# Optimization experiments

Measured on AMD Instinct MI355X. Metric: run time of the kernel, lower is better.

The kernel has to match this reference:

```python
import jax, jax.numpy as jnp
import numpy as np

V, E, H, D = 10000, 256, 512, 768  # vocab, embed, hidden(=attn), encoder dims
B, T, N = 32, 128, 196


def setup_inputs() -> dict:
    key = jax.random.key(0)
    ks = jax.random.split(key, 16)
    s = 0.02
    inp = {
        "x": jax.random.randint(ks[0], (B, T), 0, V),
        "enc_mem": jax.random.normal(ks[1], (B, N, D), dtype=jnp.float32),
        "enc_mask": jnp.ones((B, N), dtype=jnp.int32),
        # parameters, stored (in, out) so y = x @ W
        "emb_table": jax.random.normal(ks[2], (V, E), dtype=jnp.float32) * s,
        "We": jax.random.normal(ks[3], (D, H), dtype=jnp.float32) * s,   # attn.W_e
        "Wh": jax.random.normal(ks[4], (H, H), dtype=jnp.float32) * s,   # attn.W_h
        "v": jax.random.normal(ks[5], (H,), dtype=jnp.float32) * s,      # attn.v
        "Wih": jax.random.normal(ks[6], (E + D, 4 * H), dtype=jnp.float32) * s,
        "Whh": jax.random.normal(ks[7], (H, 4 * H), dtype=jnp.float32) * s,
        "bih": jnp.zeros((4 * H,), dtype=jnp.float32),
        "bhh": jnp.zeros((4 * H,), dtype=jnp.float32),
        "fcW": jax.random.normal(ks[8], (H, V), dtype=jnp.float32) * s,
        "fcb": jnp.zeros((V,), dtype=jnp.float32),
        "W2h": jax.random.normal(ks[9], (D, H), dtype=jnp.float32) * s,  # enc_to_h
        "b2h": jnp.zeros((H,), dtype=jnp.float32),
        "W2c": jax.random.normal(ks[10], (D, H), dtype=jnp.float32) * s,  # enc_to_c
        "b2c": jnp.zeros((H,), dtype=jnp.float32),
    }
    return inp


def _decode(x, enc_mem, enc_mask, emb_table, We, Wh, v, Wih, Whh, bih, bhh,
            fcW, fcb, W2h, b2h, W2c, b2c):
    emb = emb_table[x]                       # (B,T,E); dropout=0 (eval)
    pooled = enc_mem.mean(axis=1)            # (B,D)
    h = jnp.tanh(pooled @ W2h + b2h)         # init_hidden
    c = jnp.tanh(pooled @ W2c + b2c)
    Ke = jnp.einsum('bnd,dh->bnh', enc_mem, We)  # precompute W_e(enc_mem)
    neg = jnp.float32(-1e9)
    mask0 = (enc_mask == 0)

    def step(carry, e_t):
        h, c = carry
        energy = jnp.tanh((h @ Wh)[:, None, :] + Ke)        # (B,N,H)
        scores = jnp.einsum('bnh,h->bn', energy, v)         # (B,N)
        scores = jnp.where(mask0, neg, scores)
        alpha = jax.nn.softmax(scores, axis=-1)
        context = jnp.einsum('bn,bnd->bd', alpha, enc_mem)  # (B,D)
        lstm_in = jnp.concatenate([e_t, context], axis=-1)  # (B,E+D)
        gates = lstm_in @ Wih + bih + h @ Whh + bhh         # (B,4H)
        i_g, f_g, g_g, o_g = jnp.split(gates, 4, axis=-1)   # torch order i,f,g,o
        c_new = jax.nn.sigmoid(f_g) * c + jax.nn.sigmoid(i_g) * jnp.tanh(g_g)
        h_new = jax.nn.sigmoid(o_g) * jnp.tanh(c_new)
        logit = h_new @ fcW + fcb                           # (B,V)
        return (h_new, c_new), logit

    (h, c), logits_t = jax.lax.scan(step, (h, c), jnp.swapaxes(emb, 0, 1))
    logits = jnp.swapaxes(logits_t, 0, 1)                   # (B,T,V)
    return logits, h, c


def reference(x, enc_mem, enc_mask, emb_table, We, Wh, v, Wih, Whh, bih, bhh,
              fcW, fcb, W2h, b2h, W2c, b2c):
    return _decode(x, enc_mem, enc_mask, emb_table, We, Wh, v, Wih, Whh,
                   bih, bhh, fcW, fcb, W2h, b2h, W2c, b2c)
```

## Files before the change

### kernel.cpp

```cpp
#include <hip/hip_runtime.h>

typedef unsigned short u16;
typedef __attribute__((ext_vector_type(8))) short short8;
typedef __attribute__((ext_vector_type(4))) float f32x4;
typedef __attribute__((ext_vector_type(4))) unsigned int u32x4;

#define B_  32
#define T_  128
#define N_  196
#define D_  768
#define E_  256
#define H_  512
#define V_  10000
#define G4H 2048
#define NBLK 256
#define BH  (B_ * H_)
#define BD  (B_ * D_)

#define O_ENCBF 0UL
#define O_WHT   9633792UL
#define O_WHHT  10158080UL
#define O_WIHDT 12255232UL
#define O_KE    15400960UL
#define O_GEMB  21823488UL
#define O_BSUM  38600704UL
#define O_CT    38608896UL
#define O_HIST  38674432UL
#define O_HX2   42868736UL
#define O_HWX   42934272UL
#define O_CTXA  42999808UL
#define O_DEN   43196416UL
#define O_BARS  43196672UL
#define O_REL   43198720UL

__device__ __forceinline__ float b2f(u16 u) {
  union { unsigned i; float f; } c; c.i = ((unsigned)u) << 16; return c.f;
}
__device__ __forceinline__ u16 f2b(float f) {
  unsigned u = __float_as_uint(f);
  unsigned r = (u + 0x7fffu + ((u >> 16) & 1u)) >> 16;
  return (u16)r;
}
__device__ __forceinline__ float fast_tanh(float x) {
  float e = __expf(2.f * x);
  return 1.f - 2.f * __builtin_amdgcn_rcpf(e + 1.f);
}
__device__ __forceinline__ float sigm(float x) {
  return __builtin_amdgcn_rcpf(1.f + __expf(-x));
}
__device__ __forceinline__ float wred_sum(float x) {
  #pragma unroll
  for (int o = 32; o; o >>= 1) x += __shfl_xor(x, o, 64);
  return x;
}

__device__ __forceinline__ float ld_bypass_f32(const float* p) {
  float v;
  asm volatile("global_load_dword %0, %1, off sc0 sc1\n\ts_waitcnt vmcnt(0)"
               : "=v"(v) : "v"(p) : "memory");
  return v;
}
__device__ __forceinline__ unsigned ld_bypass_u32(const unsigned* p) {
  unsigned v;
  asm volatile("global_load_dword %0, %1, off sc0 sc1\n\ts_waitcnt vmcnt(0)"
               : "=v"(v) : "v"(p) : "memory");
  return v;
}
__device__ __forceinline__ void ld2_bypass(const void* p0, const void* p1,
                                           u32x4& a, u32x4& b) {
  asm volatile(
    "global_load_dwordx4 %0, %2, off sc0 sc1\n\t"
    "global_load_dwordx4 %1, %3, off sc0 sc1\n\t"
    "s_waitcnt vmcnt(0)"
    : "=&v"(a), "=&v"(b) : "v"(p0), "v"(p1) : "memory");
}
__device__ __forceinline__ void ld6_1_bypass(
    const void* p0, const void* p1, const void* p2, const void* p3,
    const void* p4, const void* p5, const void* pd,
    u32x4& a, u32x4& b, u32x4& c, u32x4& d, u32x4& e, u32x4& f, float& dv) {
  asm volatile(
    "global_load_dwordx4 %0, %7, off sc0 sc1\n\t"
    "global_load_dwordx4 %1, %8, off sc0 sc1\n\t"
    "global_load_dwordx4 %2, %9, off sc0 sc1\n\t"
    "global_load_dwordx4 %3, %10, off sc0 sc1\n\t"
    "global_load_dwordx4 %4, %11, off sc0 sc1\n\t"
    "global_load_dwordx4 %5, %12, off sc0 sc1\n\t"
    "global_load_dword %6, %13, off sc0 sc1\n\t"
    "s_waitcnt vmcnt(0)"
    : "=&v"(a), "=&v"(b), "=&v"(c), "=&v"(d), "=&v"(e), "=&v"(f), "=&v"(dv)
    : "v"(p0), "v"(p1), "v"(p2), "v"(p3), "v"(p4), "v"(p5), "v"(pd)
    : "memory");
}
__device__ __forceinline__ void st_bypass_f32(float* p, float v) {
  asm volatile("global_store_dword %0, %1, off sc0 sc1" :: "v"(p), "v"(v) : "memory");
}
__device__ __forceinline__ void st_bypass_u32(unsigned* p, unsigned v) {
  asm volatile("global_store_dword %0, %1, off sc0 sc1" :: "v"(p), "v"(v) : "memory");
}
__device__ __forceinline__ void st_bypass_u16(u16* p, u16 v) {
  unsigned vv = v;
  asm volatile("global_store_short %0, %1, off sc0 sc1" :: "v"(p), "v"(vv) : "memory");
}

__device__ __forceinline__ unsigned bar_sum16(const unsigned* p) {
  unsigned a0,a1,a2,a3,a4,a5,a6,a7,a8,a9,a10,a11,a12,a13,a14,a15;
  asm volatile(
    "global_load_dword %0, %16, off sc0 sc1\n\t"
    "global_load_dword %1, %16, off offset:128 sc0 sc1\n\t"
    "global_load_dword %2, %16, off offset:256 sc0 sc1\n\t"
    "global_load_dword %3, %16, off offset:384 sc0 sc1\n\t"
    "global_load_dword %4, %16, off offset:512 sc0 sc1\n\t"
    "global_load_dword %5, %16, off offset:640 sc0 sc1\n\t"
    "global_load_dword %6, %16, off offset:768 sc0 sc1\n\t"
    "global_load_dword %7, %16, off offset:896 sc0 sc1\n\t"
    "global_load_dword %8, %16, off offset:1024 sc0 sc1\n\t"
    "global_load_dword %9, %16, off offset:1152 sc0 sc1\n\t"
    "global_load_dword %10, %16, off offset:1280 sc0 sc1\n\t"
    "global_load_dword %11, %16, off offset:1408 sc0 sc1\n\t"
    "global_load_dword %12, %16, off offset:1536 sc0 sc1\n\t"
    "global_load_dword %13, %16, off offset:1664 sc0 sc1\n\t"
    "global_load_dword %14, %16, off offset:1792 sc0 sc1\n\t"
    "global_load_dword %15, %16, off offset:1920 sc0 sc1\n\t"
    "s_waitcnt vmcnt(0)"
    : "=&v"(a0), "=&v"(a1), "=&v"(a2), "=&v"(a3), "=&v"(a4), "=&v"(a5),
      "=&v"(a6), "=&v"(a7), "=&v"(a8), "=&v"(a9), "=&v"(a10), "=&v"(a11),
      "=&v"(a12), "=&v"(a13), "=&v"(a14), "=&v"(a15)
    : "v"(p) : "memory");
  return ((a0+a1)+(a2+a3)) + ((a4+a5)+(a6+a7)) +
         ((a8+a9)+(a10+a11)) + ((a12+a13)+(a14+a15));
}

__device__ __forceinline__ void gridbar(unsigned* bars, unsigned* rel,
                                        int bid, unsigned target) {
  __syncthreads();
  if (bid == 0) {
    if (threadIdx.x == 0) {
      asm volatile("s_waitcnt vmcnt(0) lgkmcnt(0)" ::: "memory");
      __hip_atomic_fetch_add(bars, 1u, __ATOMIC_RELAXED, __HIP_MEMORY_SCOPE_AGENT);
      while (bar_sum16(bars) < target) __builtin_amdgcn_s_sleep(1);
    }
    __syncthreads();
    if (threadIdx.x < NBLK) st_bypass_u32(rel + (size_t)threadIdx.x * 32, target);
  } else {
    if (threadIdx.x == 0) {
      asm volatile("s_waitcnt vmcnt(0) lgkmcnt(0)" ::: "memory");
      __hip_atomic_fetch_add(bars + (size_t)(bid & 15) * 32, 1u,
                             __ATOMIC_RELAXED, __HIP_MEMORY_SCOPE_AGENT);
      while (ld_bypass_u32(rel + (size_t)bid * 32) < target)
        __builtin_amdgcn_s_sleep(2);
    }
    __syncthreads();
  }
}


__global__ void conv_bf(const float* __restrict__ in, u16* __restrict__ out, int n) {
  int i = blockIdx.x * blockDim.x + threadIdx.x;
  int st = gridDim.x * blockDim.x;
  for (; i < n; i += st) out[i] = f2b(in[i]);
}

__global__ void bsum_k(const float* __restrict__ a, const float* __restrict__ b,
                       float* __restrict__ o, int n) {
  int i = blockIdx.x * blockDim.x + threadIdx.x;
  if (i < n) o[i] = a[i] + b[i];
}

__global__ void transpose_bf(const float* __restrict__ in, u16* __restrict__ out, int R, int C) {
  __shared__ float tl[64][65];
  int tid = threadIdx.x;
  int tc0 = blockIdx.x * 64, tr0 = blockIdx.y * 64;
  int cc = tid & 63;
  for (int rr = tid >> 6; rr < 64; rr += 4) {
    int rg = tr0 + rr, cg = tc0 + cc;
    tl[rr][cc] = (rg < R && cg < C) ? in[(size_t)rg * C + cg] : 0.f;
  }
  __syncthreads();
  int rr = tid & 63;
  for (int c2 = tid >> 6; c2 < 64; c2 += 4) {
    int cg = tc0 + c2, rg = tr0 + rr;
    if (cg < C && rg < R) out[(size_t)cg * R + rg] = f2b(tl[rr][c2]);
  }
}

__global__ __launch_bounds__(512) void init_hc(
    const float* __restrict__ enc, const float* __restrict__ W2h,
    const float* __restrict__ b2h, const float* __restrict__ W2c,
    const float* __restrict__ b2c, u16* __restrict__ hx2, float* __restrict__ cT)
{
  __shared__ float pool[D_];
  int b = blockIdx.x, tid = threadIdx.x;
  for (int d = tid; d < D_; d += 512) {
    float s = 0.f;
    const float* ep = enc + (size_t)b * N_ * D_ + d;
    for (int n = 0; n < N_; ++n) s += ep[(size_t)n * D_];
    pool[d] = s * (1.f / 196.f);
  }
  __syncthreads();
  float a = b2h[tid], a2 = b2c[tid];
  #pragma unroll 4
  for (int d = 0; d < D_; ++d) {
    float pv = pool[d];
    a  += pv * W2h[d * H_ + tid];
    a2 += pv * W2c[d * H_ + tid];
  }
  hx2[b * H_ + tid] = f2b(fast_tanh(a));
  cT[b * H_ + tid] = fast_tanh(a2);
}

template<int AMODE, int OUTMODE, int BIAS>
__global__ __launch_bounds__(256) void gemm2(
    const void* __restrict__ Av, const float* __restrict__ Bf,
    const int* __restrict__ xidx, void* __restrict__ Cv,
    const float* __restrict__ bias, int M, int N, int K, int lda)
{
  __shared__ __align__(16) u16 Al[128][72];
  __shared__ __align__(16) u16 Bl[128][72];
  const int tid = threadIdx.x;
  const int tm0 = blockIdx.y * 128, tn0 = blockIdx.x * 128;
  const int wv = tid >> 6, lane = tid & 63;
  const int wr = wv >> 1, wc = wv & 1;
  f32x4 acc[4][4] = {};
  const int r = tid >> 1, cb = (tid & 1) * 32;
  const int bkr = tid >> 5;
  const int bnc = (tid & 31) * 4;
  for (int k0 = 0; k0 < K; k0 += 64) {
    int rm = tm0 + r; if (rm >= M) rm = M - 1;
    if (AMODE == 0) {
      const u16* gp = (const u16*)Av + (size_t)rm * lda + k0 + cb;
      #pragma unroll
      for (int u = 0; u < 4; ++u)
        *(short8*)&Al[r][cb + u * 8] = *(const short8*)(gp + u * 8);
    } else {
      const float* gp = (const float*)Av + (size_t)xidx[rm] * lda + k0 + cb;
      #pragma unroll
      for (int u = 0; u < 4; ++u) {
        f32x4 a0 = *(const f32x4*)(gp + u * 8);
        f32x4 a1 = *(const f32x4*)(gp + u * 8 + 4);
        Al[r][cb + u * 8 + 0] = f2b(a0[0]); Al[r][cb + u * 8 + 1] = f2b(a0[1]);
        Al[r][cb + u * 8 + 2] = f2b(a0[2]); Al[r][cb + u * 8 + 3] = f2b(a0[3]);
        Al[r][cb + u * 8 + 4] = f2b(a1[0]); Al[r][cb + u * 8 + 5] = f2b(a1[1]);
        Al[r][cb + u * 8 + 6] = f2b(a1[2]); Al[r][cb + u * 8 + 7] = f2b(a1[3]);
      }
    }
    {
      int ncc = tn0 + bnc; if (ncc > N - 4) ncc = N - 4;
      #pragma unroll
      for (int u = 0; u < 8; ++u) {
        int kr = bkr + u * 8;
        const float* bp = Bf + (size_t)(k0 + kr) * N + ncc;
        f32x4 bv = *(const f32x4*)bp;
        #pragma unroll
        for (int j = 0; j < 4; ++j) Bl[bnc + j][kr] = f2b(bv[j]);
      }
    }
    __syncthreads();
    #pragma unroll
    for (int kk = 0; kk < 64; kk += 32) {
      short8 af[4], bfv[4];
      #pragma unroll
      for (int i = 0; i < 4; ++i)
        af[i] = *(const short8*)&Al[wr * 64 + i * 16 + (lane & 15)][kk + (lane >> 4) * 8];
      #pragma unroll
      for (int j = 0; j < 4; ++j)
        bfv[j] = *(const short8*)&Bl[wc * 64 + j * 16 + (lane & 15)][kk + (lane >> 4) * 8];
      #pragma unroll
      for (int i = 0; i < 4; ++i)
        #pragma unroll
        for (int j = 0; j < 4; ++j)
          acc[i][j] = __builtin_amdgcn_mfma_f32_16x16x32_bf16(af[i], bfv[j], acc[i][j], 0, 0, 0);
    }
    __syncthreads();
  }
  #pragma unroll
  for (int i = 0; i < 4; ++i) {
    int row0 = tm0 + wr * 64 + i * 16 + (lane >> 4) * 4;
    #pragma unroll
    for (int j = 0; j < 4; ++j) {
      int col = tn0 + wc * 64 + j * 16 + (lane & 15);
      if (col < N) {
        float bs = BIAS ? bias[col] : 0.f;
        #pragma unroll
        for (int rr2 = 0; rr2 < 4; ++rr2) {
          int row = row0 + rr2;
          if (row < M) {
            float val = acc[i][j][rr2] + bs;
            if (OUTMODE == 0) ((float*)Cv)[(size_t)row * N + col] = val;
            else if (OUTMODE == 1) ((u16*)Cv)[(size_t)row * N + col] = f2b(val);
            else {
              int tt = row & 127, bb = row >> 7;
              ((u16*)Cv)[((size_t)tt * G4H + col) * 32 + bb] = f2b(val);
            }
          }
        }
      }
    }
  }
}

__global__ __launch_bounds__(512, 1) void recur8(
    const u16* __restrict__ enc_bf, const int* __restrict__ mask,
    const u16* __restrict__ Ke, const u16* __restrict__ WhT,
    const float* __restrict__ vvec, const u16* __restrict__ WhhT,
    const u16* __restrict__ WihDT, const u16* __restrict__ g_emb,
    const float* __restrict__ cT0,
    u16* hx2, float* hwx, float* ctxAcc, float* denom,
    u16* h_hist, float* out_h, float* out_c, unsigned* bars, unsigned* rel)
{
  __shared__ u32x4 hst16[64 * 16];
  __shared__ union {
    struct { float hw8[512]; float e[32]; } p2;
    struct { u32x4 ctx16[96 * 16]; f32x4 part3[8][69]; } p3;
  } su;
  __shared__ float gpre[16][16];
  __shared__ float cfl[4][16];
  __shared__ float maskf[32];

  const int bid = blockIdx.x, tid = threadIdx.x;
  const int lane = tid & 63, wvx = tid >> 6;
  const int b = bid >> 3, s8 = bid & 7;
  const int n0 = s8 * 25;
  const int nmax = min(25, N_ - n0);
  const int bh = bid >> 7, hb4 = bid & 127;
  const int b_base = bh * 16, hx4 = hb4 * 4;
  const int n16 = lane & 15, kh = lane >> 4;
  const int gcol = (n16 >> 2) * H_ + hx4 + (n16 & 3);
  const bool is_hw = (bid & 3) == 0;
  const int c0 = ((bid >> 2) & 31) * 16;
  const int bl = tid & 15, kc0 = tid >> 4;
  const int ro = tid & 15, co = tid >> 4;

  float vreg[8];
  #pragma unroll
  for (int j = 0; j < 8; ++j) vreg[j] = vvec[lane * 8 + j];
  if (tid < nmax) maskf[tid] = (mask[b * N_ + n0 + tid] == 0) ? 0.f : 1.f;
  if (tid < 64) cfl[tid >> 4][tid & 15] =
      cT0[(b_base + (tid & 15)) * H_ + hx4 + (tid >> 4)];

  short8 wf[5];
  #pragma unroll
  for (int i = 0; i < 5; ++i) {
    int ks = wvx * 5 + i;
    if (ks < 16) wf[i] = *(const short8*)(WhhT + (size_t)gcol * H_ + ks * 32 + kh * 8);
    else         wf[i] = *(const short8*)(WihDT + (size_t)gcol * D_ + (ks - 16) * 32 + kh * 8);
  }
  short8 kvp[4];
  #pragma unroll
  for (int i = 0; i < 4; ++i) {
    int nn = wvx + i * 8; if (nn >= nmax) nn = nmax - 1;
    kvp[i] = *(const short8*)(Ke + ((size_t)(b * N_ + n0 + nn)) * H_ + lane * 8);
  }
  __syncthreads();

  unsigned tgt = 0;
  for (int t = 0; t < T_; ++t) {
    const int rb = t & 1, wb = rb ^ 1;
    const int cbuf = t & 1, nbuf = cbuf ^ 1;
    {
      const u16* hp = hx2 + (size_t)rb * BH + (b_base + bl) * H_;
      u32x4 v0, v1;
      ld2_bypass(hp + kc0 * 8, hp + (kc0 + 32) * 8, v0, v1);
      hst16[(kc0     ) * 16 + bl] = v0;
      hst16[(kc0 + 32) * 16 + bl] = v1;
    }
    __syncthreads();
    if (is_hw) {
      f32x4 hwacc = {0.f, 0.f, 0.f, 0.f};
      #pragma unroll
      for (int ks = 0; ks < 16; ++ks) {
        short8 bfrag = *(const short8*)(WhT + (size_t)(c0 + n16) * H_ + ks * 32 + kh * 8);
        hwacc = __builtin_amdgcn_mfma_f32_16x16x32_bf16(
            *(const short8*)&hst16[(ks * 4 + kh) * 16 + n16], bfrag, hwacc, 0, 0, 0);
      }
      #pragma unroll
      for (int j = 0; j < 4; ++j)
        st_bypass_f32(hwx + (size_t)(b_base + kh * 4 + j) * H_ + c0 + n16, hwacc[j]);
    }
    tgt += NBLK;
    f32x4 gacc = {0.f, 0.f, 0.f, 0.f};
    float ge_pf = 0.f;
    __syncthreads();
    if (tid == 0) {
      asm volatile("s_waitcnt vmcnt(0) lgkmcnt(0)" ::: "memory");
      __hip_atomic_fetch_add(bars + (size_t)(bid & 15) * 32, 1u,
                             __ATOMIC_RELAXED, __HIP_MEMORY_SCOPE_AGENT);
    }
    if (bid == 0) {
      if (tid == 0) { while (bar_sum16(bars) < tgt) __builtin_amdgcn_s_sleep(1); }
      __syncthreads();
      if (tid < NBLK) st_bypass_u32(rel + (size_t)tid * 32, tgt);
      #pragma unroll
      for (int i = 0; i < 5; ++i) {
        int ks = wvx * 5 + i;
        if (ks < 16)
          gacc = __builtin_amdgcn_mfma_f32_16x16x32_bf16(
              *(const short8*)&hst16[(ks * 4 + kh) * 16 + n16], wf[i], gacc, 0, 0, 0);
      }
      if (tid < 256) {
        int gco = (co >> 2) * H_ + hx4 + (co & 3);
        ge_pf = b2f(g_emb[((size_t)t * G4H + gco) * 32 + (b_base + ro)]);
      }
    } else {
      #pragma unroll
      for (int i = 0; i < 5; ++i) {
        int ks = wvx * 5 + i;
        if (ks < 16)
          gacc = __builtin_amdgcn_mfma_f32_16x16x32_bf16(
              *(const short8*)&hst16[(ks * 4 + kh) * 16 + n16], wf[i], gacc, 0, 0, 0);
      }
      if (tid < 256) {
        int gco = (co >> 2) * H_ + hx4 + (co & 3);
        ge_pf = b2f(g_emb[((size_t)t * G4H + gco) * 32 + (b_base + ro)]);
      }
      __syncthreads();
      if (tid == 0) {
        while (ld_bypass_u32(rel + (size_t)bid * 32) < tgt)
          __builtin_amdgcn_s_sleep(2);
      }
      __syncthreads();
    }

    su.p2.hw8[(tid & 7) * 64 + (tid >> 3)] = ld_bypass_f32(hwx + b * H_ + tid);
    __syncthreads();
    #pragma unroll
    for (int i = 0; i < 4; ++i) {
      int nn = wvx + i * 8;
      if (nn < nmax) {
        float p = 0.f;
        #pragma unroll
        for (int j = 0; j < 8; ++j)
          p += vreg[j] * fast_tanh(su.p2.hw8[j * 64 + lane] + b2f((u16)kvp[i][j]));
        p = wred_sum(p);
        if (lane == 0) su.p2.e[nn] = maskf[nn] * __expf(p);
      }
    }
    __syncthreads();
    if (wvx == 0) {
      float sp = (lane < nmax) ? su.p2.e[lane] : 0.f;
      sp = wred_sum(sp);
      if (lane == 0) atomicAdd(denom + cbuf * 32 + b, sp);
    }
    if (tid < 384) {
      float a0 = 0.f, a1 = 0.f;
      const u16* ep0 = enc_bf + ((size_t)(b * N_ + n0)) * D_ + 2 * tid;
      for (int nn = 0; nn < nmax; ++nn) {
        float ev = su.p2.e[nn];
        unsigned w = *(const unsigned*)(ep0 + (size_t)nn * D_);
        a0 += ev * b2f((u16)(w & 0xffffu));
        a1 += ev * b2f((u16)(w >> 16));
      }
      float* cp = ctxAcc + (size_t)cbuf * BD + b * D_ + 2 * tid;
      atomicAdd(cp, a0);
      atomicAdd(cp + 1, a1);
    }
    tgt += NBLK; gridbar(bars, rel, bid, tgt);

    {
      const float* cp = ctxAcc + (size_t)cbuf * BD + (size_t)(b_base + bl) * D_;
      u32x4 ca[3][2]; float dv;
      ld6_1_bypass(cp + (kc0     ) * 8, cp + (kc0     ) * 8 + 4,
                   cp + (kc0 + 32) * 8, cp + (kc0 + 32) * 8 + 4,
                   cp + (kc0 + 64) * 8, cp + (kc0 + 64) * 8 + 4,
                   denom + cbuf * 32 + (b_base + bl),
                   ca[0][0], ca[0][1], ca[1][0], ca[1][1],
                   ca[2][0], ca[2][1], dv);
      float rdv = 1.f / dv;
      #pragma unroll
      for (int r2 = 0; r2 < 3; ++r2) {
        int kc = kc0 + r2 * 32;
        u32x4 pk;
        #pragma unroll
        for (int hh = 0; hh < 2; ++hh) {
          float x0 = __uint_as_float(ca[r2][hh][0]) * rdv;
          float x1 = __uint_as_float(ca[r2][hh][1]) * rdv;
          float x2 = __uint_as_float(ca[r2][hh][2]) * rdv;
          float x3 = __uint_as_float(ca[r2][hh][3]) * rdv;
          pk[hh * 2]     = (unsigned)f2b(x0) | ((unsigned)f2b(x1) << 16);
          pk[hh * 2 + 1] = (unsigned)f2b(x2) | ((unsigned)f2b(x3) << 16);
        }
        su.p3.ctx16[kc * 16 + bl] = pk;
      }
    }
    __syncthreads();
    #pragma unroll
    for (int i = 0; i < 5; ++i) {
      int ks = wvx * 5 + i;
      if (ks >= 16)
        gacc = __builtin_amdgcn_mfma_f32_16x16x32_bf16(
            *(const short8*)&su.p3.ctx16[((ks - 16) * 4 + kh) * 16 + n16], wf[i],
            gacc, 0, 0, 0);
    }
    *(f32x4*)&su.p3.part3[wvx][lane] = gacc;
    __syncthreads();
    if (tid < 256) {
      int lp = ((ro >> 2) << 4) | co;
      float v = su.p3.part3[0][lp][ro & 3] + su.p3.part3[1][lp][ro & 3]
              + su.p3.part3[2][lp][ro & 3] + su.p3.part3[3][lp][ro & 3]
              + su.p3.part3[4][lp][ro & 3] + su.p3.part3[5][lp][ro & 3]
              + su.p3.part3[6][lp][ro & 3] + su.p3.part3[7][lp][ro & 3];
      gpre[co][ro] = v + ge_pf;
    }
    __syncthreads();
    if (tid < 64) {
      int row = tid & 15, j = tid >> 4;
      float gI = gpre[j][row], gF = gpre[4 + j][row];
      float gG = gpre[8 + j][row], gO = gpre[12 + j][row];
      float co2 = cfl[j][row];
      float cn = sigm(gF) * co2 + sigm(gI) * fast_tanh(gG);
      float hn = sigm(gO) * fast_tanh(cn);
      cfl[j][row] = cn;
      int bgl = b_base + row, hidx = hx4 + j;
      st_bypass_u16(hx2 + (size_t)wb * BH + bgl * H_ + hidx, f2b(hn));
      h_hist[((size_t)(bgl * T_ + t)) * H_ + hidx] = f2b(hn);
      if (t == T_ - 1) {
        out_h[bgl * H_ + hidx] = hn;
        out_c[bgl * H_ + hidx] = cn;
      }
    }
    tgt += NBLK;
    __syncthreads();
    if (tid == 0) {
      asm volatile("s_waitcnt vmcnt(0) lgkmcnt(0)" ::: "memory");
      __hip_atomic_fetch_add(bars + (size_t)(bid & 15) * 32, 1u,
                             __ATOMIC_RELAXED, __HIP_MEMORY_SCOPE_AGENT);
    }
    if (bid == 0) {
      if (tid == 0) { while (bar_sum16(bars) < tgt) __builtin_amdgcn_s_sleep(1); }
      __syncthreads();
      if (tid < NBLK) st_bypass_u32(rel + (size_t)tid * 32, tgt);
      if (tid < 96) st_bypass_f32(ctxAcc + (size_t)nbuf * BD + bid * 96 + tid, 0.f);
      if (tid < 32) st_bypass_f32(denom + nbuf * 32 + tid, 0.f);
    } else {
      if (tid < 96) st_bypass_f32(ctxAcc + (size_t)nbuf * BD + bid * 96 + tid, 0.f);
      __syncthreads();
      if (tid == 0) {
        while (ld_bypass_u32(rel + (size_t)bid * 32) < tgt)
          __builtin_amdgcn_s_sleep(2);
      }
      __syncthreads();
    }
  }
}

extern "C" void kernel_launch(void* const* d_in, const int* in_sizes, int n_in,
                              void* d_out, int out_size, void* d_ws, size_t ws_size,
                              hipStream_t stream) {
  const int*   x    = (const int*)d_in[0];
  const float* enc  = (const float*)d_in[1];
  const int*   mask = (const int*)d_in[2];
  const float* emb  = (const float*)d_in[3];
  const float* We   = (const float*)d_in[4];
  const float* Wh   = (const float*)d_in[5];
  const float* v    = (const float*)d_in[6];
  const float* Wih  = (const float*)d_in[7];
  const float* Whh  = (const float*)d_in[8];
  const float* bih  = (const float*)d_in[9];
  const float* bhh  = (const float*)d_in[10];
  const float* fcW  = (const float*)d_in[11];
  const float* fcb  = (const float*)d_in[12];
  const float* W2h  = (const float*)d_in[13];
  const float* b2h  = (const float*)d_in[14];
  const float* W2c  = (const float*)d_in[15];
  const float* b2c  = (const float*)d_in[16];
  float* out = (float*)d_out;

  char* ws = (char*)d_ws;
  u16* enc_bf = (u16*)(ws + O_ENCBF);
  u16* WhT    = (u16*)(ws + O_WHT);
  u16* WhhT   = (u16*)(ws + O_WHHT);
  u16* WihDT  = (u16*)(ws + O_WIHDT);
  u16* Ke     = (u16*)(ws + O_KE);
  u16* g_emb  = (u16*)(ws + O_GEMB);
  float* bsum = (float*)(ws + O_BSUM);
  float* cT   = (float*)(ws + O_CT);
  u16* h_hist = (u16*)(ws + O_HIST);
  u16* hx2    = (u16*)(ws + O_HX2);
  float* hwx  = (float*)(ws + O_HWX);
  float* ctxAcc = (float*)(ws + O_CTXA);
  float* denom  = (float*)(ws + O_DEN);
  unsigned* bars = (unsigned*)(ws + O_BARS);
  unsigned* rel  = (unsigned*)(ws + O_REL);
  float* out_h = out + (size_t)B_ * T_ * V_;
  float* out_c = out_h + B_ * H_;

  hipMemsetAsync(bars, 0, 2048, stream);
  hipMemsetAsync(rel, 0, 32768, stream);
  hipMemsetAsync(ctxAcc, 0, 196608, stream);
  hipMemsetAsync(denom, 0, 256, stream);
  conv_bf<<<1024, 256, 0, stream>>>(enc, enc_bf, B_ * N_ * D_);
  transpose_bf<<<dim3(8, 8), 256, 0, stream>>>(Wh, WhT, H_, H_);
  transpose_bf<<<dim3(32, 8), 256, 0, stream>>>(Whh, WhhT, H_, G4H);
  transpose_bf<<<dim3(32, 12), 256, 0, stream>>>(Wih + (size_t)E_ * G4H, WihDT, D_, G4H);
  bsum_k<<<8, 256, 0, stream>>>(bih, bhh, bsum, G4H);
  init_hc<<<32, 512, 0, stream>>>(enc, W2h, b2h, W2c, b2c, hx2, cT);
  gemm2<0, 1, 0><<<dim3(4, 49), 256, 0, stream>>>(enc_bf, We, nullptr, (void*)Ke,
                                                  nullptr, B_ * N_, H_, D_, D_);
  gemm2<1, 3, 1><<<dim3(16, 32), 256, 0, stream>>>(emb, Wih, x, (void*)g_emb,
                                                   bsum, B_ * T_, G4H, E_, E_);
  recur8<<<NBLK, 512, 0, stream>>>(enc_bf, mask, Ke, WhT, v, WhhT, WihDT, g_emb,
                                   cT, hx2, hwx, ctxAcc, denom,
                                   h_hist, out_h, out_c, bars, rel);
  gemm2<0, 0, 1><<<dim3(79, 32), 256, 0, stream>>>(h_hist, fcW, nullptr, (void*)out,
                                                   fcb, B_ * T_, V_, H_, H_);
}
```

Baseline: 2.642 ms.

## Spread h@Wh across all blocks with register-resident weights; unroll context loop

Previously only one in four blocks computed h@Wh with MFMA, reloading WhT fragments from global memory every step. Now every block computes a 16x4 slice of h@Wh on plain FP32 lanes, with its WhT slice kept in registers for all steps, and reduces the partial sums through shared memory. The context accumulation loop is fully unrolled to a fixed 25 iterations, with clamped row indices and zero-padded attention weights standing in for the variable trip count. The cost is more registers per thread and an extra shared-memory reduction and barrier on every timestep.

```diff
diff --git a/kernel.cpp b/kernel.cpp
--- a/kernel.cpp
+++ b/kernel.cpp
@@ -298,7 +298,7 @@
   }
 }
 
-__global__ __launch_bounds__(512, 1) void recur8(
+__global__ __launch_bounds__(512, 1) void recur9(
     const u16* __restrict__ enc_bf, const int* __restrict__ mask,
     const u16* __restrict__ Ke, const u16* __restrict__ WhT,
     const float* __restrict__ vvec, const u16* __restrict__ WhhT,
@@ -309,6 +309,7 @@
 {
   __shared__ u32x4 hst16[64 * 16];
   __shared__ union {
+    struct { float part1[8][64]; } p1;
     struct { float hw8[512]; float e[32]; } p2;
     struct { u32x4 ctx16[96 * 16]; f32x4 part3[8][69]; } p3;
   } su;
@@ -325,8 +326,8 @@
   const int b_base = bh * 16, hx4 = hb4 * 4;
   const int n16 = lane & 15, kh = lane >> 4;
   const int gcol = (n16 >> 2) * H_ + hx4 + (n16 & 3);
-  const bool is_hw = (bid & 3) == 0;
-  const int c0 = ((bid >> 2) & 31) * 16;
+  const int hb16 = tid & 15, hc4 = (tid >> 4) & 3, hks = tid >> 6;
+  const int hwc = hb4 * 4 + hc4;
   const int bl = tid & 15, kc0 = tid >> 4;
   const int ro = tid & 15, co = tid >> 4;
 
@@ -344,6 +345,10 @@
     if (ks < 16) wf[i] = *(const short8*)(WhhT + (size_t)gcol * H_ + ks * 32 + kh * 8);
     else         wf[i] = *(const short8*)(WihDT + (size_t)gcol * D_ + (ks - 16) * 32 + kh * 8);
   }
+  short8 wh8[8];
+  #pragma unroll
+  for (int i = 0; i < 8; ++i)
+    wh8[i] = *(const short8*)(WhT + (size_t)hwc * H_ + hks * 64 + i * 8);
   short8 kvp[4];
   #pragma unroll
   for (int i = 0; i < 4; ++i) {
@@ -364,17 +369,23 @@
       hst16[(kc0 + 32) * 16 + bl] = v1;
     }
     __syncthreads();
-    if (is_hw) {
-      f32x4 hwacc = {0.f, 0.f, 0.f, 0.f};
-      #pragma unroll
-      for (int ks = 0; ks < 16; ++ks) {
-        short8 bfrag = *(const short8*)(WhT + (size_t)(c0 + n16) * H_ + ks * 32 + kh * 8);
-        hwacc = __builtin_amdgcn_mfma_f32_16x16x32_bf16(
-            *(const short8*)&hst16[(ks * 4 + kh) * 16 + n16], bfrag, hwacc, 0, 0, 0);
-      }
-      #pragma unroll
-      for (int j = 0; j < 4; ++j)
-        st_bypass_f32(hwx + (size_t)(b_base + kh * 4 + j) * H_ + c0 + n16, hwacc[j]);
+    {
+      float acc = 0.f;
+      #pragma unroll
+      for (int i = 0; i < 8; ++i) {
+        short8 hb8 = *(const short8*)&hst16[(hks * 8 + i) * 16 + hb16];
+        #pragma unroll
+        for (int j = 0; j < 8; ++j)
+          acc += b2f((u16)wh8[i][j]) * b2f((u16)hb8[j]);
+      }
+      su.p1.part1[hks][hc4 * 16 + hb16] = acc;
+    }
+    __syncthreads();
+    if (tid < 64) {
+      float s = 0.f;
+      #pragma unroll
+      for (int w = 0; w < 8; ++w) s += su.p1.part1[w][tid];
+      st_bypass_f32(hwx + (size_t)(b_base + (tid & 15)) * H_ + hb4 * 4 + (tid >> 4), s);
     }
     tgt += NBLK;
     f32x4 gacc = {0.f, 0.f, 0.f, 0.f};
@@ -421,6 +432,7 @@
     }
 
     su.p2.hw8[(tid & 7) * 64 + (tid >> 3)] = ld_bypass_f32(hwx + b * H_ + tid);
+    if (tid >= 25 && tid < 32) su.p2.e[tid] = 0.f;
     __syncthreads();
     #pragma unroll
     for (int i = 0; i < 4; ++i) {
@@ -436,16 +448,18 @@
     }
     __syncthreads();
     if (wvx == 0) {
-      float sp = (lane < nmax) ? su.p2.e[lane] : 0.f;
+      float sp = (lane < 25) ? su.p2.e[lane] : 0.f;
       sp = wred_sum(sp);
       if (lane == 0) atomicAdd(denom + cbuf * 32 + b, sp);
     }
     if (tid < 384) {
       float a0 = 0.f, a1 = 0.f;
       const u16* ep0 = enc_bf + ((size_t)(b * N_ + n0)) * D_ + 2 * tid;
-      for (int nn = 0; nn < nmax; ++nn) {
+      #pragma unroll
+      for (int nn = 0; nn < 25; ++nn) {
+        int nn_c = (nn < nmax) ? nn : 0;
         float ev = su.p2.e[nn];
-        unsigned w = *(const unsigned*)(ep0 + (size_t)nn * D_);
+        unsigned w = *(const unsigned*)(ep0 + (size_t)nn_c * D_);
         a0 += ev * b2f((u16)(w & 0xffffu));
         a1 += ev * b2f((u16)(w >> 16));
       }
@@ -597,7 +611,7 @@
                                                   nullptr, B_ * N_, H_, D_, D_);
   gemm2<1, 3, 1><<<dim3(16, 32), 256, 0, stream>>>(emb, Wih, x, (void*)g_emb,
                                                    bsum, B_ * T_, G4H, E_, E_);
-  recur8<<<NBLK, 512, 0, stream>>>(enc_bf, mask, Ke, WhT, v, WhhT, WihDT, g_emb,
+  recur9<<<NBLK, 512, 0, stream>>>(enc_bf, mask, Ke, WhT, v, WhhT, WihDT, g_emb,
                                    cT, hx2, hwx, ctxAcc, denom,
                                    h_hist, out_h, out_c, bars, rel);
   gemm2<0, 0, 1><<<dim3(79, 32), 256, 0, stream>>>(h_hist, fcW, nullptr, (void*)out,
```

New measurement: 2.512 ms. -4.9%, faster.
